# Kernel tuning notes

Hardware: AMD Instinct MI355X
Metric: run time of the kernel (lower is better)

The kernel has to match this reference:

```python
import jax, jax.numpy as jnp
import numpy as np

NUM_BUCKETS = 64
MAX_DISTANCE = 50000.0


def setup_inputs() -> dict:
    R, I, N, E, H = 64, 512, 4, 256, 8
    key = jax.random.key(0)
    ks = jax.random.split(key, 12)
    p = lambda k, shape: (jax.random.normal(k, shape, dtype=jnp.float32) * 0.02)
    return {
        "x": jax.random.normal(ks[0], (R, I, N, E), dtype=jnp.float32),
        "distances": jax.random.randint(ks[1], (N, I, I), 0, 50000).astype(jnp.int32),
        "Wq": p(ks[2], (E, E)), "bq": jnp.zeros((E,), jnp.float32),
        "Wk": p(ks[3], (E, E)), "bk": jnp.zeros((E,), jnp.float32),
        "Wv": p(ks[4], (E, E)), "bv": jnp.zeros((E,), jnp.float32),
        "Wo": p(ks[5], (E, E)), "bo": jnp.zeros((E,), jnp.float32),
        "rel_emb": p(ks[6], (NUM_BUCKETS, H)),
    }


def reference(x, distances, Wq, bq, Wk, bk, Wv, bv, Wo, bo, rel_emb):
    R, I, N, E = x.shape
    H = rel_emb.shape[1]
    D = E // H
    # scaling = head_dim**-0.5 / sqrt(num_rows)
    scaling = (D ** -0.5) / np.sqrt(R)

    def proj(W, b):
        return (jnp.einsum('rine,fe->rinf', x, W) + b).reshape(R, I, N, H, D)

    q = proj(Wq, bq) * scaling
    k = proj(Wk, bk)
    v = proj(Wv, bv)

    # Row-summed attention logits: (H, N, I, J)
    attn_weights = jnp.einsum('rinhd,rjnhd->hnij', q, k)

    # T5-style relative position bias (buckets = linspace boundaries)
    buckets = jnp.linspace(0.0, MAX_DISTANCE, NUM_BUCKETS - 1)
    abs_dist = jnp.abs(distances).astype(jnp.float32)
    # torch.bucketize(right=False) == searchsorted side='left'
    bucket_idx = jnp.searchsorted(buckets, abs_dist, side='left')  # (N, I, J)
    bias = rel_emb[bucket_idx]                  # (N, I, J, H)
    attn_weights = attn_weights + jnp.transpose(bias, (3, 0, 1, 2))

    attn_probs = jax.nn.softmax(attn_weights, axis=-1)  # dropout p=0.0 -> identity

    context = jnp.einsum('hnij,rjnhd->rinhd', attn_probs, v).reshape(R, I, N, E)
    output = jnp.einsum('rine,fe->rinf', context, Wo) + bo
    return output, attn_probs
```

## Files before the change

kernel.cpp:

```cpp
#include <hip/hip_runtime.h>

typedef unsigned short u16;
typedef unsigned int u32;
typedef float f32x4 __attribute__((ext_vector_type(4)));
typedef short bf16x8 __attribute__((ext_vector_type(8)));
typedef unsigned short u16x8 __attribute__((ext_vector_type(8)));

#define SL 33554432u

__device__ __forceinline__ float bf2f(u16 u) {
  u32 v = ((u32)u) << 16;
  return __builtin_bit_cast(float, v);
}
__device__ __forceinline__ u16 f2bf(float f) {
  u32 i = __builtin_bit_cast(u32, f);
  i += 0x7fffu + ((i >> 16) & 1u);
  return (u16)(i >> 16);
}

#define GLDS16(g, l) __builtin_amdgcn_global_load_lds( \
    (const __attribute__((address_space(1))) void*)(g), \
    (__attribute__((address_space(3))) void*)(l), 16, 0, 0)

__device__ __forceinline__ void stage128(const u16* gbase, int ldk, u16* lds, int tid) {
  #pragma unroll
  for (int rep = 0; rep < 4; ++rep) {
    int c = tid + rep * 256;
    int row = c >> 3, slot = c & 7;
    const u16* g = gbase + (size_t)row * ldk + ((slot ^ (row & 7)) << 3);
    GLDS16(g, lds + c * 8);
  }
}

__device__ __forceinline__ void mfma128(const u16* As, const u16* Bs, int lane,
                                        int wm0, int wn0, f32x4 acc[4][4]) {
  #pragma unroll
  for (int kk = 0; kk < 2; ++kk) {
    bf16x8 a[4], b[4];
    #pragma unroll
    for (int mi = 0; mi < 4; ++mi) {
      int r = wm0 + mi * 16 + (lane & 15);
      int c16 = (kk * 4 + (lane >> 4)) ^ (r & 7);
      a[mi] = *(const bf16x8*)(As + r * 64 + c16 * 8);
    }
    #pragma unroll
    for (int ni = 0; ni < 4; ++ni) {
      int r = wn0 + ni * 16 + (lane & 15);
      int c16 = (kk * 4 + (lane >> 4)) ^ (r & 7);
      b[ni] = *(const bf16x8*)(Bs + r * 64 + c16 * 8);
    }
    #pragma unroll
    for (int mi = 0; mi < 4; ++mi)
      #pragma unroll
      for (int ni = 0; ni < 4; ++ni)
        acc[mi][ni] = __builtin_amdgcn_mfma_f32_16x16x32_bf16(a[mi], b[ni], acc[mi][ni], 0, 0, 0);
  }
}

__device__ __forceinline__ void gemm_core(const u16* A, int ldkA, const u16* B, int ldkB,
                                          int NT, u16* As, u16* Bs,
                                          int tid, int lane, int wm0, int wn0,
                                          f32x4 acc[4][4]) {
  for (int t = 0; t < NT; ++t) {
    stage128(A + t * 64, ldkA, As, tid);
    stage128(B + t * 64, ldkB, Bs, tid);
    __syncthreads();
    mfma128(As, Bs, lane, wm0, wn0, acc);
    __syncthreads();
  }
}

__global__ __launch_bounds__(256) void k_castx(const float* __restrict__ src,
                                               u16* __restrict__ dst) {
  int idx = blockIdx.x * 256 + threadIdx.x;
  const float4* s = (const float4*)src;
  float4 a = s[(size_t)idx * 2], b = s[(size_t)idx * 2 + 1];
  u16x8 o;
  o[0] = f2bf(a.x); o[1] = f2bf(a.y); o[2] = f2bf(a.z); o[3] = f2bf(a.w);
  o[4] = f2bf(b.x); o[5] = f2bf(b.y); o[6] = f2bf(b.z); o[7] = f2bf(b.w);
  *(u16x8*)(dst + (size_t)idx * 8) = o;
}

__global__ __launch_bounds__(256) void k_castw(
    const float* __restrict__ Wq, const float* __restrict__ Wk,
    const float* __restrict__ Wv, const float* __restrict__ Wo,
    u16* __restrict__ Wb) {
  int idx = blockIdx.x * 256 + threadIdx.x;
  int w = idx >> 13, off = idx & 8191;
  const float* src = (w == 0) ? Wq : (w == 1) ? Wk : (w == 2) ? Wv : Wo;
  const float4* s = (const float4*)(src + (size_t)off * 8);
  float4 a = s[0], b = s[1];
  u16x8 o;
  o[0] = f2bf(a.x); o[1] = f2bf(a.y); o[2] = f2bf(a.z); o[3] = f2bf(a.w);
  o[4] = f2bf(b.x); o[5] = f2bf(b.y); o[6] = f2bf(b.z); o[7] = f2bf(b.w);
  *(u16x8*)(Wb + (size_t)w * 65536 + (size_t)off * 8) = o;
}

__global__ __launch_bounds__(256) void k_proj_mm(
    const u16* __restrict__ xb, const u16* __restrict__ Wb,
    const float* __restrict__ bq, const float* __restrict__ bk, const float* __restrict__ bv,
    u16* __restrict__ qt, u16* __restrict__ kt, u16* __restrict__ vt, float scaling) {
  __shared__ __align__(16) u16 As[128 * 64];
  __shared__ __align__(16) u16 Bs[128 * 64];
  const int tid = threadIdx.x, lane = tid & 63, wave = tid >> 6;
  const int wm0 = (wave >> 1) * 64, wn0 = (wave & 1) * 64;
  const int bid = blockIdx.x;
  const int sb = (bid & 7) * 768 + (bid >> 3);
  const int mt = sb / 6, g = sb % 6;
  const int m0 = mt * 128, n0 = (g & 1) * 128, w = g >> 1;

  f32x4 acc[4][4];
  #pragma unroll
  for (int mi = 0; mi < 4; ++mi)
    #pragma unroll
    for (int ni = 0; ni < 4; ++ni) acc[mi][ni] = (f32x4){0.f, 0.f, 0.f, 0.f};

  gemm_core(xb + (size_t)m0 * 256, 256, Wb + w * 65536 + (size_t)n0 * 256, 256,
            4, As, Bs, tid, lane, wm0, wn0, acc);

  const float* bias = (w == 0) ? bq : (w == 1) ? bk : bv;
  u16* dst = (w == 0) ? qt : (w == 1) ? kt : vt;
  const float sc = (w == 0) ? scaling : 1.0f;

  #pragma unroll
  for (int mi = 0; mi < 4; ++mi)
    #pragma unroll
    for (int ni = 0; ni < 4; ++ni) {
      int f = n0 + wn0 + ni * 16 + (lane & 15);
      int h = f >> 5, d = f & 31;
      float bb = bias[f];
      #pragma unroll
      for (int q = 0; q < 4; ++q) {
        int m = m0 + wm0 + mi * 16 + (lane >> 4) * 4 + q;
        int n = m & 3, i = (m >> 2) & 511, r = m >> 11;
        size_t o = ((size_t)((n * 8 + h) * 512 + i)) * 2048 + r * 32 + d;
        dst[o] = f2bf((acc[mi][ni][q] + bb) * sc);
      }
    }
}

__global__ __launch_bounds__(256) void k_attn_mm(
    const u16* __restrict__ qt, const u16* __restrict__ kt, u16* __restrict__ lgt) {
  __shared__ __align__(16) u16 As[128 * 64];
  __shared__ __align__(16) u16 Bs[128 * 64];
  const int tid = threadIdx.x, lane = tid & 63, wave = tid >> 6;
  const int wm0 = (wave >> 1) * 64, wn0 = (wave & 1) * 64;
  const int bid = blockIdx.x;
  const int sb = (bid & 7) * 64 + (bid >> 3);
  const int nh = sb >> 4, tt = sb & 15;
  const int m0 = (tt >> 2) * 128, n0 = (tt & 3) * 128;

  f32x4 acc[4][4];
  #pragma unroll
  for (int mi = 0; mi < 4; ++mi)
    #pragma unroll
    for (int ni = 0; ni < 4; ++ni) acc[mi][ni] = (f32x4){0.f, 0.f, 0.f, 0.f};

  const size_t base = (size_t)nh * 512 * 2048;
  gemm_core(qt + base + (size_t)m0 * 2048, 2048, kt + base + (size_t)n0 * 2048, 2048,
            32, As, Bs, tid, lane, wm0, wn0, acc);

  #pragma unroll
  for (int mi = 0; mi < 4; ++mi)
    #pragma unroll
    for (int ni = 0; ni < 4; ++ni) {
      int col = n0 + wn0 + ni * 16 + (lane & 15);
      #pragma unroll
      for (int q = 0; q < 4; ++q) {
        int row = m0 + wm0 + mi * 16 + (lane >> 4) * 4 + q;
        lgt[(size_t)nh * 262144 + (size_t)row * 512 + col] = f2bf(acc[mi][ni][q]);
      }
    }
}

__global__ __launch_bounds__(256) void k_softmax(
    const u16* __restrict__ lgt, const int* __restrict__ dist, const float* __restrict__ rel,
    float* __restrict__ probs, u16* __restrict__ pbf) {
  const int t = threadIdx.x;
  const int lane = t & 63, wv = t >> 6;
  const int b = blockIdx.x;
  const int i = b & 511, n = b >> 9;

  const int* dr = dist + ((size_t)n * 512 + i) * 512 + lane * 8;
  int4 dA = *(const int4*)dr, dB = *(const int4*)(dr + 4);
  int dd[8] = {dA.x, dA.y, dA.z, dA.w, dB.x, dB.y, dB.z, dB.w};
  int u[8];
  #pragma unroll
  for (int j = 0; j < 8; ++j) {
    int v = dd[j] < 0 ? -dd[j] : dd[j];
    int q = (62 * v + 49999) / 50000; if (q > 63) q = 63;
    u[j] = q;
  }

  #pragma unroll
  for (int hh = 0; hh < 2; ++hh) {
    const int h = wv * 2 + hh;
    const int nh = n * 8 + h;
    const u16* lr = lgt + ((size_t)nh * 512 + i) * 512 + lane * 8;
    u16x8 L = *(const u16x8*)lr;
    float vj[8];
    float mx = -1e30f;
    #pragma unroll
    for (int j = 0; j < 8; ++j) {
      vj[j] = bf2f(L[j]) + rel[u[j] * 8 + h];
      mx = fmaxf(mx, vj[j]);
    }
    #pragma unroll
    for (int off = 32; off; off >>= 1) mx = fmaxf(mx, __shfl_xor(mx, off));
    float s = 0.f;
    #pragma unroll
    for (int j = 0; j < 8; ++j) { vj[j] = __expf(vj[j] - mx); s += vj[j]; }
    #pragma unroll
    for (int off = 32; off; off >>= 1) s += __shfl_xor(s, off);
    float inv = 1.0f / s;
    float4 pa, pb;
    pa.x = vj[0]*inv; pa.y = vj[1]*inv; pa.z = vj[2]*inv; pa.w = vj[3]*inv;
    pb.x = vj[4]*inv; pb.y = vj[5]*inv; pb.z = vj[6]*inv; pb.w = vj[7]*inv;
    size_t po = ((size_t)(h * 4 + n) * 512 + i) * 512 + lane * 8;
    *(float4*)(probs + po) = pa;
    *(float4*)(probs + po + 4) = pb;
    u16x8 pc;
    pc[0]=f2bf(pa.x); pc[1]=f2bf(pa.y); pc[2]=f2bf(pa.z); pc[3]=f2bf(pa.w);
    pc[4]=f2bf(pb.x); pc[5]=f2bf(pb.y); pc[6]=f2bf(pb.z); pc[7]=f2bf(pb.w);
    size_t pq = ((size_t)nh * 512 + i) * 512 + lane * 8;
    *(u16x8*)(pbf + pq) = pc;
  }
}

__global__ __launch_bounds__(256) void k_vtrans(const u16* __restrict__ vt, u16* __restrict__ vtt) {
  __shared__ u16 ts[64][72];
  const int b = blockIdx.x;
  const int ct_ = b & 31, it = (b >> 5) & 7, nh = b >> 8;
  const int i0 = it * 64, c0 = ct_ * 64;
  const int t = threadIdx.x;
  #pragma unroll
  for (int rep = 0; rep < 2; ++rep) {
    int c = t + rep * 256;
    int r = c >> 3, q = c & 7;
    u16x8 v = *(const u16x8*)(vt + ((size_t)nh * 512 + i0 + r) * 2048 + c0 + q * 8);
    #pragma unroll
    for (int j = 0; j < 8; ++j) ts[r][q * 8 + j] = v[j];
  }
  __syncthreads();
  #pragma unroll
  for (int rep = 0; rep < 2; ++rep) {
    int c = t + rep * 256;
    int rr = c >> 3, q = c & 7;
    u16x8 o;
    #pragma unroll
    for (int j = 0; j < 8; ++j) o[j] = ts[q * 8 + j][rr];
    *(u16x8*)(vtt + ((size_t)nh * 2048 + c0 + rr) * 512 + i0 + q * 8) = o;
  }
}

__global__ __launch_bounds__(256) void k_ctx_mm(
    const u16* __restrict__ vtt, const u16* __restrict__ pbf, u16* __restrict__ ct) {
  __shared__ __align__(16) u16 lds[16640];
  u16* As = lds;
  u16* Bs = lds + 8192;
  u16* ts = lds;
  const int tid = threadIdx.x, lane = tid & 63, wave = tid >> 6;
  const int wm0 = (wave >> 1) * 64, wn0 = (wave & 1) * 64;
  const int bid = blockIdx.x;
  const int sb = (bid & 7) * 256 + (bid >> 3);
  const int nh = sb >> 6, tt = sb & 63;
  const int m0 = (tt >> 2) * 128, n0 = (tt & 3) * 128;
  const int n = nh >> 3, h = nh & 7;

  f32x4 acc[4][4];
  #pragma unroll
  for (int mi = 0; mi < 4; ++mi)
    #pragma unroll
    for (int ni = 0; ni < 4; ++ni) acc[mi][ni] = (f32x4){0.f, 0.f, 0.f, 0.f};

  gemm_core(vtt + (size_t)nh * 1048576 + (size_t)m0 * 512, 512,
            pbf + (size_t)nh * 262144 + (size_t)n0 * 512, 512,
            8, As, Bs, tid, lane, wm0, wn0, acc);

  #pragma unroll
  for (int mi = 0; mi < 4; ++mi)
    #pragma unroll
    for (int ni = 0; ni < 4; ++ni) {
      int i_l = wn0 + ni * 16 + (lane & 15);
      #pragma unroll
      for (int q = 0; q < 4; ++q) {
        int c_l = wm0 + mi * 16 + (lane >> 4) * 4 + q;
        ts[i_l * 130 + c_l] = f2bf(acc[mi][ni][q]);
      }
    }
  __syncthreads();
  #pragma unroll
  for (int cc = 0; cc < 2; ++cc) {
    int ch = tid + cc * 256;
    int i_l = ch & 127, r_l = ch >> 7;
    const u16* src = ts + i_l * 130 + r_l * 32;
    int rr = (m0 >> 5) + r_l;
    size_t o = ((size_t)((rr * 512 + n0 + i_l) * 4 + n)) * 256 + h * 32;
    #pragma unroll
    for (int j = 0; j < 4; ++j)
      *(u16x8*)(ct + o + j * 8) = *(const u16x8*)(src + j * 8);
  }
}

__global__ __launch_bounds__(256) void k_oproj_mm(
    const u16* __restrict__ ct, const u16* __restrict__ Wob,
    const float* __restrict__ bo, float* __restrict__ out) {
  __shared__ __align__(16) u16 As[128 * 64];
  __shared__ __align__(16) u16 Bs[128 * 64];
  const int tid = threadIdx.x, lane = tid & 63, wave = tid >> 6;
  const int wm0 = (wave >> 1) * 64, wn0 = (wave & 1) * 64;
  const int bid = blockIdx.x;
  const int sb = (bid & 7) * 256 + (bid >> 3);
  const int m0 = (sb >> 1) * 128, n0 = (sb & 1) * 128;

  f32x4 acc[4][4];
  #pragma unroll
  for (int mi = 0; mi < 4; ++mi)
    #pragma unroll
    for (int ni = 0; ni < 4; ++ni) acc[mi][ni] = (f32x4){0.f, 0.f, 0.f, 0.f};

  gemm_core(ct + (size_t)m0 * 256, 256, Wob + (size_t)n0 * 256, 256,
            4, As, Bs, tid, lane, wm0, wn0, acc);

  #pragma unroll
  for (int mi = 0; mi < 4; ++mi)
    #pragma unroll
    for (int ni = 0; ni < 4; ++ni) {
      int col = n0 + wn0 + ni * 16 + (lane & 15);
      float bb = bo[col];
      #pragma unroll
      for (int q = 0; q < 4; ++q) {
        int row = m0 + wm0 + mi * 16 + (lane >> 4) * 4 + q;
        out[(size_t)row * 256 + col] = acc[mi][ni][q] + bb;
      }
    }
}

extern "C" void kernel_launch(void* const* d_in, const int* in_sizes, int n_in,
                              void* d_out, int out_size, void* d_ws, size_t ws_size,
                              hipStream_t stream) {
  const float* x  = (const float*)d_in[0];
  const int* dist = (const int*)d_in[1];
  const float* Wq = (const float*)d_in[2];
  const float* bq = (const float*)d_in[3];
  const float* Wk = (const float*)d_in[4];
  const float* bk = (const float*)d_in[5];
  const float* Wv = (const float*)d_in[6];
  const float* bv = (const float*)d_in[7];
  const float* Wo = (const float*)d_in[8];
  const float* bo = (const float*)d_in[9];
  const float* rel = (const float*)d_in[10];
  float* out = (float*)d_out;
  float* probs = out + (size_t)SL;

  u16* ws = (u16*)d_ws;
  u16* xb  = ws;
  u16* qt  = ws + (size_t)SL;
  u16* kt  = ws + (size_t)2 * SL;
  u16* vt  = ws + (size_t)3 * SL;
  u16* lgt = xb;
  u16* pbf = qt;
  u16* vtt = kt;
  u16* ctb = xb;
  u16* Wb  = ws + (size_t)4 * SL;

  const float scaling = 0.022097086912079608f;

  k_castx  <<<16384, 256, 0, stream>>>(x, xb);
  k_castw  <<<128, 256, 0, stream>>>(Wq, Wk, Wv, Wo, Wb);
  k_proj_mm<<<6144, 256, 0, stream>>>(xb, Wb, bq, bk, bv, qt, kt, vt, scaling);
  k_attn_mm<<<512, 256, 0, stream>>>(qt, kt, lgt);
  k_softmax<<<2048, 256, 0, stream>>>(lgt, dist, rel, probs, pbf);
  k_vtrans <<<8192, 256, 0, stream>>>(vt, vtt);
  k_ctx_mm <<<2048, 256, 0, stream>>>(vtt, pbf, ctb);
  k_oproj_mm<<<2048, 256, 0, stream>>>(ctb, Wb + 196608, bo, out);
}
```

Baseline: 337.7 us.

## Swap MFMA operands to vectorize GEMM epilogue stores, drop ctx LDS transpose

```diff
diff --git a/kernel.cpp b/kernel.cpp
--- a/kernel.cpp
+++ b/kernel.cpp
@@ -32,6 +32,7 @@
   }
 }
 
+template <bool SWAP>
 __device__ __forceinline__ void mfma128(const u16* As, const u16* Bs, int lane,
                                         int wm0, int wn0, f32x4 acc[4][4]) {
   #pragma unroll
@@ -53,10 +54,13 @@
     for (int mi = 0; mi < 4; ++mi)
       #pragma unroll
       for (int ni = 0; ni < 4; ++ni)
-        acc[mi][ni] = __builtin_amdgcn_mfma_f32_16x16x32_bf16(a[mi], b[ni], acc[mi][ni], 0, 0, 0);
-  }
-}
-
+        acc[mi][ni] = SWAP
+          ? __builtin_amdgcn_mfma_f32_16x16x32_bf16(b[ni], a[mi], acc[mi][ni], 0, 0, 0)
+          : __builtin_amdgcn_mfma_f32_16x16x32_bf16(a[mi], b[ni], acc[mi][ni], 0, 0, 0);
+  }
+}
+
+template <bool SWAP>
 __device__ __forceinline__ void gemm_core(const u16* A, int ldkA, const u16* B, int ldkB,
                                           int NT, u16* As, u16* Bs,
                                           int tid, int lane, int wm0, int wn0,
@@ -65,7 +69,7 @@
     stage128(A + t * 64, ldkA, As, tid);
     stage128(B + t * 64, ldkB, Bs, tid);
     __syncthreads();
-    mfma128(As, Bs, lane, wm0, wn0, acc);
+    mfma128<SWAP>(As, Bs, lane, wm0, wn0, acc);
     __syncthreads();
   }
 }
@@ -104,10 +108,7 @@
   __shared__ __align__(16) u16 Bs[128 * 64];
   const int tid = threadIdx.x, lane = tid & 63, wave = tid >> 6;
   const int wm0 = (wave >> 1) * 64, wn0 = (wave & 1) * 64;
-  const int bid = blockIdx.x;
-  const int sb = (bid & 7) * 768 + (bid >> 3);
-  const int mt = sb / 6, g = sb % 6;
-  const int m0 = mt * 128, n0 = (g & 1) * 128, w = g >> 1;
+  const int m0 = blockIdx.x * 128, n0 = blockIdx.y * 128, w = blockIdx.z;
 
   f32x4 acc[4][4];
   #pragma unroll
@@ -115,28 +116,31 @@
     #pragma unroll
     for (int ni = 0; ni < 4; ++ni) acc[mi][ni] = (f32x4){0.f, 0.f, 0.f, 0.f};
 
-  gemm_core(xb + (size_t)m0 * 256, 256, Wb + w * 65536 + (size_t)n0 * 256, 256,
-            4, As, Bs, tid, lane, wm0, wn0, acc);
+  gemm_core<true>(xb + (size_t)m0 * 256, 256, Wb + w * 65536 + (size_t)n0 * 256, 256,
+                  4, As, Bs, tid, lane, wm0, wn0, acc);
 
   const float* bias = (w == 0) ? bq : (w == 1) ? bk : bv;
   u16* dst = (w == 0) ? qt : (w == 1) ? kt : vt;
   const float sc = (w == 0) ? scaling : 1.0f;
 
   #pragma unroll
-  for (int mi = 0; mi < 4; ++mi)
-    #pragma unroll
-    for (int ni = 0; ni < 4; ++ni) {
-      int f = n0 + wn0 + ni * 16 + (lane & 15);
-      int h = f >> 5, d = f & 31;
-      float bb = bias[f];
-      #pragma unroll
-      for (int q = 0; q < 4; ++q) {
-        int m = m0 + wm0 + mi * 16 + (lane >> 4) * 4 + q;
-        int n = m & 3, i = (m >> 2) & 511, r = m >> 11;
-        size_t o = ((size_t)((n * 8 + h) * 512 + i)) * 2048 + r * 32 + d;
-        dst[o] = f2bf((acc[mi][ni][q] + bb) * sc);
-      }
-    }
+  for (int ni = 0; ni < 4; ++ni) {
+    int f = n0 + wn0 + ni * 16 + (lane >> 4) * 4;
+    int h = f >> 5, d = f & 31;
+    float4 bb = *(const float4*)(bias + f);
+    #pragma unroll
+    for (int mi = 0; mi < 4; ++mi) {
+      int m = m0 + wm0 + mi * 16 + (lane & 15);
+      int n = m & 3, i = (m >> 2) & 511, r = m >> 11;
+      size_t o = ((size_t)((n * 8 + h) * 512 + i)) * 2048 + r * 32 + d;
+      ushort4 wv4;
+      wv4.x = f2bf((acc[mi][ni][0] + bb.x) * sc);
+      wv4.y = f2bf((acc[mi][ni][1] + bb.y) * sc);
+      wv4.z = f2bf((acc[mi][ni][2] + bb.z) * sc);
+      wv4.w = f2bf((acc[mi][ni][3] + bb.w) * sc);
+      *(ushort4*)(dst + o) = wv4;
+    }
+  }
 }
 
 __global__ __launch_bounds__(256) void k_attn_mm(
@@ -157,20 +161,23 @@
     for (int ni = 0; ni < 4; ++ni) acc[mi][ni] = (f32x4){0.f, 0.f, 0.f, 0.f};
 
   const size_t base = (size_t)nh * 512 * 2048;
-  gemm_core(qt + base + (size_t)m0 * 2048, 2048, kt + base + (size_t)n0 * 2048, 2048,
-            32, As, Bs, tid, lane, wm0, wn0, acc);
-
-  #pragma unroll
-  for (int mi = 0; mi < 4; ++mi)
+  gemm_core<true>(qt + base + (size_t)m0 * 2048, 2048, kt + base + (size_t)n0 * 2048, 2048,
+                  32, As, Bs, tid, lane, wm0, wn0, acc);
+
+  #pragma unroll
+  for (int mi = 0; mi < 4; ++mi) {
+    int row = m0 + wm0 + mi * 16 + (lane & 15);
     #pragma unroll
     for (int ni = 0; ni < 4; ++ni) {
-      int col = n0 + wn0 + ni * 16 + (lane & 15);
-      #pragma unroll
-      for (int q = 0; q < 4; ++q) {
-        int row = m0 + wm0 + mi * 16 + (lane >> 4) * 4 + q;
-        lgt[(size_t)nh * 262144 + (size_t)row * 512 + col] = f2bf(acc[mi][ni][q]);
-      }
-    }
+      int col = n0 + wn0 + ni * 16 + (lane >> 4) * 4;
+      ushort4 wv4;
+      wv4.x = f2bf(acc[mi][ni][0]);
+      wv4.y = f2bf(acc[mi][ni][1]);
+      wv4.z = f2bf(acc[mi][ni][2]);
+      wv4.w = f2bf(acc[mi][ni][3]);
+      *(ushort4*)(lgt + (size_t)nh * 262144 + (size_t)row * 512 + col) = wv4;
+    }
+  }
 }
 
 __global__ __launch_bounds__(256) void k_softmax(
@@ -255,10 +262,8 @@
 
 __global__ __launch_bounds__(256) void k_ctx_mm(
     const u16* __restrict__ vtt, const u16* __restrict__ pbf, u16* __restrict__ ct) {
-  __shared__ __align__(16) u16 lds[16640];
-  u16* As = lds;
-  u16* Bs = lds + 8192;
-  u16* ts = lds;
+  __shared__ __align__(16) u16 As[128 * 64];
+  __shared__ __align__(16) u16 Bs[128 * 64];
   const int tid = threadIdx.x, lane = tid & 63, wave = tid >> 6;
   const int wm0 = (wave >> 1) * 64, wn0 = (wave & 1) * 64;
   const int bid = blockIdx.x;
@@ -273,32 +278,25 @@
     #pragma unroll
     for (int ni = 0; ni < 4; ++ni) acc[mi][ni] = (f32x4){0.f, 0.f, 0.f, 0.f};
 
-  gemm_core(vtt + (size_t)nh * 1048576 + (size_t)m0 * 512, 512,
-            pbf + (size_t)nh * 262144 + (size_t)n0 * 512, 512,
-            8, As, Bs, tid, lane, wm0, wn0, acc);
-
-  #pragma unroll
-  for (int mi = 0; mi < 4; ++mi)
+  gemm_core<false>(vtt + (size_t)nh * 1048576 + (size_t)m0 * 512, 512,
+                   pbf + (size_t)nh * 262144 + (size_t)n0 * 512, 512,
+                   8, As, Bs, tid, lane, wm0, wn0, acc);
+
+  #pragma unroll
+  for (int mi = 0; mi < 4; ++mi) {
+    int c_g = m0 + wm0 + mi * 16 + (lane >> 4) * 4;
+    int rr = c_g >> 5, d = c_g & 31;
     #pragma unroll
     for (int ni = 0; ni < 4; ++ni) {
-      int i_l = wn0 + ni * 16 + (lane & 15);
-      #pragma unroll
-      for (int q = 0; q < 4; ++q) {
-        int c_l = wm0 + mi * 16 + (lane >> 4) * 4 + q;
-        ts[i_l * 130 + c_l] = f2bf(acc[mi][ni][q]);
-      }
-    }
-  __syncthreads();
-  #pragma unroll
-  for (int cc = 0; cc < 2; ++cc) {
-    int ch = tid + cc * 256;
-    int i_l = ch & 127, r_l = ch >> 7;
-    const u16* src = ts + i_l * 130 + r_l * 32;
-    int rr = (m0 >> 5) + r_l;
-    size_t o = ((size_t)((rr * 512 + n0 + i_l) * 4 + n)) * 256 + h * 32;
-    #pragma unroll
-    for (int j = 0; j < 4; ++j)
-      *(u16x8*)(ct + o + j * 8) = *(const u16x8*)(src + j * 8);
+      int i_g = n0 + wn0 + ni * 16 + (lane & 15);
+      size_t o = ((size_t)((rr * 512 + i_g) * 4 + n)) * 256 + h * 32 + d;
+      ushort4 wv4;
+      wv4.x = f2bf(acc[mi][ni][0]);
+      wv4.y = f2bf(acc[mi][ni][1]);
+      wv4.z = f2bf(acc[mi][ni][2]);
+      wv4.w = f2bf(acc[mi][ni][3]);
+      *(ushort4*)(ct + o) = wv4;
+    }
   }
 }
 
@@ -319,21 +317,24 @@
     #pragma unroll
     for (int ni = 0; ni < 4; ++ni) acc[mi][ni] = (f32x4){0.f, 0.f, 0.f, 0.f};
 
-  gemm_core(ct + (size_t)m0 * 256, 256, Wob + (size_t)n0 * 256, 256,
-            4, As, Bs, tid, lane, wm0, wn0, acc);
-
-  #pragma unroll
-  for (int mi = 0; mi < 4; ++mi)
-    #pragma unroll
-    for (int ni = 0; ni < 4; ++ni) {
-      int col = n0 + wn0 + ni * 16 + (lane & 15);
-      float bb = bo[col];
-      #pragma unroll
-      for (int q = 0; q < 4; ++q) {
-        int row = m0 + wm0 + mi * 16 + (lane >> 4) * 4 + q;
-        out[(size_t)row * 256 + col] = acc[mi][ni][q] + bb;
-      }
-    }
+  gemm_core<true>(ct + (size_t)m0 * 256, 256, Wob + (size_t)n0 * 256, 256,
+                  4, As, Bs, tid, lane, wm0, wn0, acc);
+
+  #pragma unroll
+  for (int ni = 0; ni < 4; ++ni) {
+    int col = n0 + wn0 + ni * 16 + (lane >> 4) * 4;
+    float4 bb = *(const float4*)(bo + col);
+    #pragma unroll
+    for (int mi = 0; mi < 4; ++mi) {
+      int row = m0 + wm0 + mi * 16 + (lane & 15);
+      float4 wv4;
+      wv4.x = acc[mi][ni][0] + bb.x;
+      wv4.y = acc[mi][ni][1] + bb.y;
+      wv4.z = acc[mi][ni][2] + bb.z;
+      wv4.w = acc[mi][ni][3] + bb.w;
+      *(float4*)(out + (size_t)row * 256 + col) = wv4;
+    }
+  }
 }
 
 extern "C" void kernel_launch(void* const* d_in, const int* in_sizes, int n_in,
@@ -368,7 +369,7 @@
 
   k_castx  <<<16384, 256, 0, stream>>>(x, xb);
   k_castw  <<<128, 256, 0, stream>>>(Wq, Wk, Wv, Wo, Wb);
-  k_proj_mm<<<6144, 256, 0, stream>>>(xb, Wb, bq, bk, bv, qt, kt, vt, scaling);
+  k_proj_mm<<<dim3(1024, 2, 3), 256, 0, stream>>>(xb, Wb, bq, bk, bv, qt, kt, vt, scaling);
   k_attn_mm<<<512, 256, 0, stream>>>(qt, kt, lgt);
   k_softmax<<<2048, 256, 0, stream>>>(lgt, dist, rel, probs, pbf);
   k_vtrans <<<8192, 256, 0, stream>>>(vt, vtt);
```

Measured after the change: 367.4 us. +8.8%, slower.
